# Performance work log

Measured on AMD Instinct MI355X. Metric: run time of the kernel, lower is better.

Reference implementation:

```python
import jax, jax.numpy as jnp
import numpy as np
from jax import lax

B = 65536

def _conv3(x, w, b):
    # x: [B,Cin,H,W], w: [Cout,Cin,3,3] (OIHW), SAME padding, stride 1
    y = lax.conv_general_dilated(x, w, (1, 1), 'SAME',
                                 dimension_numbers=('NCHW', 'OIHW', 'NCHW'))
    return y + b[None, :, None, None]

def _gru_cell(x, h, wu, bu, wr, br, wo, bo):
    s = jnp.concatenate([x, h], axis=1)
    update = jax.nn.sigmoid(_conv3(s, wu, bu))
    reset = jax.nn.sigmoid(_conv3(s, wr, br))
    out = jnp.tanh(_conv3(jnp.concatenate([x, h * reset], axis=1), wo, bo))
    return h * (1.0 - update) + out * update

def _mk_cell_params(key, cin, ch):
    ks = jax.random.split(key, 6)
    fan = (cin + ch) * 9
    sc = 1.0 / np.sqrt(fan)
    p = {}
    for i, g in enumerate(['u', 'r', 'o']):
        p['w' + g] = jax.random.normal(ks[2 * i], (ch, cin + ch, 3, 3), jnp.float32) * sc
        p['b' + g] = jax.random.normal(ks[2 * i + 1], (ch,), jnp.float32) * sc
    return p

def setup_inputs() -> dict:
    key = jax.random.key(0)
    k_in, k1, k2, k3, kd1, kd2 = jax.random.split(key, 6)
    inputs = jax.random.normal(k_in, (B, 1, 3, 3), jnp.float32)
    p1 = _mk_cell_params(k1, 1, 32)
    p2 = _mk_cell_params(k2, 32, 64)
    p3 = _mk_cell_params(k3, 64, 16)
    wd = jax.random.normal(kd1, (9, 16 * 3 * 3), jnp.float32) * (1.0 / 12.0)
    bd = jax.random.normal(kd2, (9,), jnp.float32) * (1.0 / 12.0)
    out = {'inputs': inputs, 'wd': wd, 'bd': bd}
    for i, p in enumerate([p1, p2, p3], start=1):
        for k, v in p.items():
            out[f'{k[0]}{i}{k[1]}'] = v  # e.g. w1u, b1u
    return out

def reference(inputs, wd, bd,
              w1u, b1u, w1r, b1r, w1o, b1o,
              w2u, b2u, w2r, b2r, w2o, b2o,
              w3u, b3u, w3r, b3r, w3o, b3o):
    b = inputs.shape[0]
    h1 = jnp.zeros((b, 32, 3, 3), inputs.dtype)
    h2 = jnp.zeros((b, 64, 3, 3), inputs.dtype)
    h3 = jnp.zeros((b, 16, 3, 3), inputs.dtype)
    x1 = _gru_cell(inputs, h1, w1u, b1u, w1r, b1r, w1o, b1o)
    x2 = _gru_cell(x1, h2, w2u, b2u, w2r, b2r, w2o, b2o)
    x3 = _gru_cell(x2, h3, w3u, b3u, w3r, b3r, w3o, b3o)
    out = x3.reshape(b, -1) @ wd.T + bd
    return (out, x1, x2, x3)
```

## Files before the change

### kernel.cpp

```cpp
#include <hip/hip_runtime.h>

#define BATCH 65536

typedef __attribute__((ext_vector_type(8))) short bf16x8;
typedef __attribute__((ext_vector_type(4))) float f32x4;

__device__ __forceinline__ unsigned short f2bf(float f) {
  unsigned int u = __float_as_uint(f);
  u += 0x7fffu + ((u >> 16) & 1u);
  return (unsigned short)(u >> 16);
}
__device__ __forceinline__ unsigned pack_trunc(float lo, float hi) {
  return __builtin_amdgcn_perm(__float_as_uint(hi), __float_as_uint(lo), 0x07060302u);
}

__device__ __forceinline__ float gru_act(float u, float o) {
  u = fmaxf(u, -60.0f);
  o = fmaxf(o, -30.0f);
  float a  = __expf(-u);
  float a2 = __expf(-2.0f * o);
  return (1.0f - a2) * __builtin_amdgcn_rcpf((1.0f + a) * (1.0f + a2));
}

__device__ __forceinline__ float conv_tap(const float* __restrict__ w, int co, int ci,
                                          int p, int q, int CINTOT) {
  int pi = p / 3, pj = p % 3, qi = q / 3, qj = q % 3;
  int di = qi - pi + 1, dj = qj - pj + 1;
  if ((unsigned)di < 3u && (unsigned)dj < 3u)
    return w[((co * CINTOT + ci) * 3 + di) * 3 + dj];
  return 0.0f;
}

__global__ void build_bt(const float* __restrict__ wu, const float* __restrict__ wo,
                         unsigned short* __restrict__ BT, int COUT, int CINX, int CINTOT) {
  int NG = COUT * 9, K = CINX * 9;
  int total = 2 * NG * K;
  int e = blockIdx.x * 256 + threadIdx.x;
  if (e >= total) return;
  int g = e / (NG * K);
  int rem = e - g * (NG * K);
  int n = rem / K, k = rem - n * K;
  BT[e] = f2bf(conv_tap(g ? wo : wu, n / 9, k / 9, n % 9, k % 9, CINTOT));
}

__global__ void build_bt1(const float* __restrict__ wu, const float* __restrict__ wo,
                          unsigned short* __restrict__ BT1) {
  int e = blockIdx.x * 256 + threadIdx.x;
  if (e >= 18432) return;
  int g = e / 9216;
  int rem = e - g * 9216;
  int n = rem / 32, k = rem - n * 32;
  float v = (k < 9) ? conv_tap(g ? wo : wu, n / 9, 0, n % 9, k, 33) : 0.0f;
  BT1[e] = f2bf(v);
}

#define OFF_X1L 0
#define OFF_X3L 0
#define OFF_WL 20480
#define OFF_BLB 25664
#define OFF_BL 40960
#define OFF_XL2 65536
#define OFF_AL 65536
#define SMEM_BYTES 74752

__global__ __launch_bounds__(256, 2) void megafused(
    const float* __restrict__ xin, const unsigned short* __restrict__ BT1,
    const float* __restrict__ b1u, const float* __restrict__ b1o,
    const unsigned short* __restrict__ BT2,
    const float* __restrict__ b2u, const float* __restrict__ b2o,
    const unsigned short* __restrict__ BT3,
    const float* __restrict__ b3u, const float* __restrict__ b3o,
    const float* __restrict__ wd, const float* __restrict__ bd,
    float* __restrict__ x1, float* __restrict__ x2,
    float* __restrict__ x3, float* __restrict__ out) {
  __shared__ __align__(16) char smem[SMEM_BYTES];
  char* x1l = smem + OFF_X1L;
  char* Bl = smem + OFF_BL;
  char* Al = smem + OFF_AL;
  unsigned short* x3l = (unsigned short*)(smem + OFF_X3L);
  float* xl2 = (float*)(smem + OFF_XL2);
  float* wl = (float*)(smem + OFF_WL);
  float* blb = (float*)(smem + OFF_BLB);

  const int tid = threadIdx.x;
  const int lane = tid & 63;
  const int wid = tid >> 6;
  const int lrow = lane & 15;
  const int jc = lane >> 4;
  const int r0 = blockIdx.x * 64;
  const int srow = tid >> 2, spart = tid & 3;

  unsigned toffB2[6];
  int wOffB2[6];
#pragma unroll
  for (int ci = 0; ci < 6; ++ci) {
    int row = ci * 64 + srow;
    int bg = (row < 192) ? row : (384 + row);
    toffB2[ci] = (unsigned)bg * 288u + spart * 8;
    wOffB2[ci] = row * 64 + ((spart ^ ((row >> 1) & 3)) << 4);
  }
  unsigned toffB1[5];
  int wOffG[5];
#pragma unroll
  for (int j = 0; j < 5; ++j) {
    int c = j * 256 + tid;
    if (c < 1152) {
      int row = c >> 2, p = c & 3;
      int g = row >= 144, nloc = row - (g ? 144 : 0);
      toffB1[j] = (unsigned)(g * 288 + nloc) * 32u + p * 8;
      wOffG[j] = row * 64 + ((p ^ ((row >> 1) & 3)) << 4);
    } else {
      toffB1[j] = 0; wOffG[j] = 0;
    }
  }

  for (int c = tid; c < 2304; c += 256) {
    int row = c / 36, col = c - row * 36;
    xl2[c] = (col < 9) ? xin[(size_t)(r0 + row) * 9 + col] : 0.0f;
  }
  bf16x8 pb[5];
#pragma unroll
  for (int j = 0; j < 5; ++j)
    if (j * 256 + tid < 1152) pb[j] = *(const bf16x8*)(BT1 + toffB1[j]);
  __syncthreads();

  bf16x8 afx[4];
#pragma unroll
  for (int m = 0; m < 4; ++m) {
    const float* xr = xl2 + (m * 16 + lrow) * 36 + jc * 8;
    float4 a0 = *(const float4*)xr;
    float4 a1 = *(const float4*)(xr + 4);
    union { uint4 u; bf16x8 v; } cv;
    cv.u.x = pack_trunc(a0.x, a0.y);
    cv.u.y = pack_trunc(a0.z, a0.w);
    cv.u.z = pack_trunc(a1.x, a1.y);
    cv.u.w = pack_trunc(a1.z, a1.w);
    afx[m] = cv.v;
  }
  int rBoffG[2][3];
#pragma unroll
  for (int g = 0; g < 2; ++g)
#pragma unroll
    for (int f = 0; f < 3; ++f) {
      int rb = g * 144 + (wid * 3 + f) * 16 + lrow;
      rBoffG[g][f] = rb * 64 + ((jc ^ ((rb >> 1) & 3)) << 4);
    }

  bf16x8 pf[6];
#pragma unroll
  for (int ch = 0; ch < 2; ++ch) {
#pragma unroll
    for (int j = 0; j < 5; ++j)
      if (j * 256 + tid < 1152) *(bf16x8*)(Bl + wOffG[j]) = pb[j];
    if (ch == 0) {
#pragma unroll
      for (int j = 0; j < 5; ++j)
        if (j * 256 + tid < 1152) pb[j] = *(const bf16x8*)(BT1 + 4608u + toffB1[j]);
    } else {
#pragma unroll
      for (int q = 0; q < 6; ++q) pf[q] = *(const bf16x8*)(BT2 + toffB2[q]);
    }
    __syncthreads();
    if (wid < 3) {
      f32x4 acc[4][2][3] = {};
      bf16x8 bfr[2][3];
#pragma unroll
      for (int g = 0; g < 2; ++g)
#pragma unroll
        for (int f = 0; f < 3; ++f) bfr[g][f] = *(const bf16x8*)(Bl + rBoffG[g][f]);
#pragma unroll
      for (int m = 0; m < 4; ++m)
#pragma unroll
        for (int g = 0; g < 2; ++g)
#pragma unroll
          for (int f = 0; f < 3; ++f)
            acc[m][g][f] = __builtin_amdgcn_mfma_f32_16x16x32_bf16(
                afx[m], bfr[g][f], acc[m][g][f], 0, 0, 0);
#pragma unroll
      for (int m = 0; m < 4; ++m)
#pragma unroll
        for (int f = 0; f < 3; ++f) {
          int n = ch * 144 + (wid * 3 + f) * 16 + lrow;
          float bU = b1u[n / 9], bO = b1o[n / 9];
          f32x4 uv = acc[m][0][f], ov = acc[m][1][f];
#pragma unroll
          for (int t = 0; t < 4; ++t) {
            int r = m * 16 + jc * 4 + t;
            float v = gru_act(uv[t] + bU, ov[t] + bO);
            x1[(size_t)(r0 + r) * 288 + n] = v;
            *(unsigned short*)(x1l + r * 640 + (((n >> 3) ^ (r & 7)) << 4) + (n & 7) * 2) =
                (unsigned short)(__float_as_uint(v) >> 16);
          }
        }
    }
    __syncthreads();
  }

  {
    int rBoff[2][3];
#pragma unroll
    for (int g = 0; g < 2; ++g)
#pragma unroll
      for (int f = 0; f < 3; ++f) {
        int rb = g * 192 + (wid * 3 + f) * 16 + lrow;
        rBoff[g][f] = rb * 64 + ((jc ^ ((rb >> 1) & 3)) << 4);
      }
    const char* aBase[4];
    int aXor[4];
#pragma unroll
    for (int m = 0; m < 4; ++m) {
      int row = m * 16 + lrow;
      aBase[m] = x1l + row * 640;
      aXor[m] = row & 7;
    }

    f32x4 acc[4][2][3] = {};
    for (int s = 0; s < 27; ++s) {
      const int kt = s - (s / 9) * 9;
#pragma unroll
      for (int ci = 0; ci < 6; ++ci) *(bf16x8*)(Bl + wOffB2[ci]) = pf[ci];
      __syncthreads();
      if (s < 26) {
        int ns = s + 1;
        unsigned uoff = (unsigned)(ns / 9) * 55296u + (unsigned)(ns % 9) * 32u;
#pragma unroll
        for (int ci = 0; ci < 6; ++ci)
          pf[ci] = *(const bf16x8*)(BT2 + uoff + toffB2[ci]);
      }
      bf16x8 af[4];
      const int c8 = kt * 4 + jc;
#pragma unroll
      for (int m = 0; m < 4; ++m)
        af[m] = *(const bf16x8*)(aBase[m] + ((c8 ^ aXor[m]) << 4));
      bf16x8 bfr[2][3];
#pragma unroll
      for (int g = 0; g < 2; ++g)
#pragma unroll
        for (int f = 0; f < 3; ++f) bfr[g][f] = *(const bf16x8*)(Bl + rBoff[g][f]);
#pragma unroll
      for (int m = 0; m < 4; ++m)
#pragma unroll
        for (int g = 0; g < 2; ++g)
#pragma unroll
          for (int f = 0; f < 3; ++f)
            acc[m][g][f] = __builtin_amdgcn_mfma_f32_16x16x32_bf16(
                af[m], bfr[g][f], acc[m][g][f], 0, 0, 0);
      if (kt == 8) {
        const int n0 = (s / 9) * 192;
#pragma unroll
        for (int m = 0; m < 4; ++m)
#pragma unroll
          for (int f = 0; f < 3; ++f) {
            int n = n0 + (wid * 3 + f) * 16 + lrow;
            float bU = b2u[n / 9], bO = b2o[n / 9];
            f32x4 uv = acc[m][0][f], ov = acc[m][1][f];
#pragma unroll
            for (int t = 0; t < 4; ++t) {
              int r = r0 + m * 16 + jc * 4 + t;
              x2[(size_t)r * 576 + n] = gru_act(uv[t] + bU, ov[t] + bO);
            }
            acc[m][0][f] = (f32x4){0.f, 0.f, 0.f, 0.f};
            acc[m][1][f] = (f32x4){0.f, 0.f, 0.f, 0.f};
          }
      }
      __syncthreads();
    }
  }
  __syncthreads();

  for (int c = tid; c < 1296; c += 256) wl[c] = wd[c];
  if (tid < 9) blb[tid] = bd[tid];

  {
    unsigned toffB3[5];
#pragma unroll
    for (int j = 0; j < 5; ++j) {
      int c = j * 256 + tid;
      toffB3[j] = (c < 1152) ? ((unsigned)(c >> 2) * 576u + (c & 3) * 8) : 0u;
    }
    const float* pA = x2 + (size_t)(r0 + srow) * 576 + spart * 8;
    char* wAl = Al + srow * 64 + ((spart ^ ((srow >> 1) & 3)) << 4);

    float4 pa0 = *(const float4*)pA;
    float4 pa1 = *(const float4*)(pA + 4);
    bf16x8 pb3[5];
#pragma unroll
    for (int j = 0; j < 5; ++j)
      if (j * 256 + tid < 1152) pb3[j] = *(const bf16x8*)(BT3 + toffB3[j]);

    const char* rA3[4];
#pragma unroll
    for (int m = 0; m < 4; ++m) {
      int row = m * 16 + lrow;
      rA3[m] = Al + row * 64 + ((jc ^ ((row >> 1) & 3)) << 4);
    }

    f32x4 acc[4][2][3] = {};
    for (int kt = 0; kt < 18; ++kt) {
      uint4 h;
      h.x = pack_trunc(pa0.x, pa0.y);
      h.y = pack_trunc(pa0.z, pa0.w);
      h.z = pack_trunc(pa1.x, pa1.y);
      h.w = pack_trunc(pa1.z, pa1.w);
      *(uint4*)wAl = h;
#pragma unroll
      for (int j = 0; j < 5; ++j)
        if (j * 256 + tid < 1152) *(bf16x8*)(Bl + wOffG[j]) = pb3[j];
      __syncthreads();
      if (kt < 17) {
        const float* gp = pA + (kt + 1) * 32;
        pa0 = *(const float4*)gp;
        pa1 = *(const float4*)(gp + 4);
        unsigned uoff = (unsigned)(kt + 1) * 32u;
#pragma unroll
        for (int j = 0; j < 5; ++j)
          if (j * 256 + tid < 1152) pb3[j] = *(const bf16x8*)(BT3 + uoff + toffB3[j]);
      }
      if (wid < 3) {
        bf16x8 af[4];
#pragma unroll
        for (int m = 0; m < 4; ++m) af[m] = *(const bf16x8*)rA3[m];
        bf16x8 bfr[2][3];
#pragma unroll
        for (int g = 0; g < 2; ++g)
#pragma unroll
          for (int f = 0; f < 3; ++f) bfr[g][f] = *(const bf16x8*)(Bl + rBoffG[g][f]);
#pragma unroll
        for (int m = 0; m < 4; ++m)
#pragma unroll
          for (int g = 0; g < 2; ++g)
#pragma unroll
            for (int f = 0; f < 3; ++f)
              acc[m][g][f] = __builtin_amdgcn_mfma_f32_16x16x32_bf16(
                  af[m], bfr[g][f], acc[m][g][f], 0, 0, 0);
      }
      __syncthreads();
    }
    if (wid < 3) {
#pragma unroll
      for (int m = 0; m < 4; ++m)
#pragma unroll
        for (int f = 0; f < 3; ++f) {
          int n = (wid * 3 + f) * 16 + lrow;
          float bU = b3u[n / 9], bO = b3o[n / 9];
          f32x4 uv = acc[m][0][f], ov = acc[m][1][f];
#pragma unroll
          for (int t = 0; t < 4; ++t) {
            int r = m * 16 + jc * 4 + t;
            float v = gru_act(uv[t] + bU, ov[t] + bO);
            x3[(size_t)(r0 + r) * 144 + n] = v;
            x3l[r * 146 + n] = (unsigned short)(__float_as_uint(v) >> 16);
          }
        }
    }
  }
  __syncthreads();

  if (wid < 3) {
    int drow = lane;
    int jb = wid * 3;
    float s0 = blb[jb], s1 = blb[jb + 1], s2 = blb[jb + 2];
    for (int k = 0; k < 144; k += 2) {
      unsigned pr = *(const unsigned*)&x3l[drow * 146 + k];
      float v0 = __uint_as_float(pr << 16);
      float v1 = __uint_as_float(pr & 0xffff0000u);
      const float2 w0 = *(const float2*)&wl[jb * 144 + k];
      const float2 w1 = *(const float2*)&wl[(jb + 1) * 144 + k];
      const float2 w2 = *(const float2*)&wl[(jb + 2) * 144 + k];
      s0 = fmaf(v0, w0.x, s0); s0 = fmaf(v1, w0.y, s0);
      s1 = fmaf(v0, w1.x, s1); s1 = fmaf(v1, w1.y, s1);
      s2 = fmaf(v0, w2.x, s2); s2 = fmaf(v1, w2.y, s2);
    }
    size_t ob = (size_t)(r0 + drow) * 9 + jb;
    out[ob] = s0; out[ob + 1] = s1; out[ob + 2] = s2;
  }
}

extern "C" void kernel_launch(void* const* d_in, const int* in_sizes, int n_in,
                              void* d_out, int out_size, void* d_ws, size_t ws_size,
                              hipStream_t stream) {
  const float* inputs = (const float*)d_in[0];
  const float* wd  = (const float*)d_in[1];
  const float* bd  = (const float*)d_in[2];
  const float* w1u = (const float*)d_in[3];
  const float* b1u = (const float*)d_in[4];
  const float* w1o = (const float*)d_in[7];
  const float* b1o = (const float*)d_in[8];
  const float* w2u = (const float*)d_in[9];
  const float* b2u = (const float*)d_in[10];
  const float* w2o = (const float*)d_in[13];
  const float* b2o = (const float*)d_in[14];
  const float* w3u = (const float*)d_in[15];
  const float* b3u = (const float*)d_in[16];
  const float* w3o = (const float*)d_in[19];
  const float* b3o = (const float*)d_in[20];

  float* out = (float*)d_out;
  float* x1 = out + (size_t)BATCH * 9;
  float* x2 = x1 + (size_t)BATCH * 288;
  float* x3 = x2 + (size_t)BATCH * 576;

  unsigned short* BT2 = (unsigned short*)d_ws;
  unsigned short* BT3 = BT2 + 331776;
  unsigned short* BT1 = BT3 + 165888;

  build_bt<<<1296, 256, 0, stream>>>(w2u, w2o, BT2, 64, 32, 96);
  build_bt<<<648, 256, 0, stream>>>(w3u, w3o, BT3, 16, 64, 80);
  build_bt1<<<72, 256, 0, stream>>>(w1u, w1o, BT1);

  megafused<<<BATCH / 64, 256, 0, stream>>>(inputs, BT1, b1u, b1o, BT2, b2u, b2o,
                                            BT3, b3u, b3o, wd, bd, x1, x2, x3, out);
}
```

Measured before the change: 154.8 us.

## Load layer-2/3 MFMA operands straight from global into registers, drop LDS staging

Layers 2 and 3 now have each wave load its B-fragments (and for layer 3 its A-fragments from x2) directly from global memory into registers. Double-buffered register sets stand in for the cooperative LDS staging, so the per-step __syncthreads barriers go away and the loop is manually unrolled by two. This removes LDS write/read traffic and block-wide sync on every k-step, and shrinks shared memory use. In exchange each wave issues redundant global loads that rely on cache hits, register pressure rises, and layer 3 reads x2 rows again from global memory.

Measured after the change: 187.0 us. 20.8% more time.

```diff
diff --git a/kernel.cpp b/kernel.cpp
--- a/kernel.cpp
+++ b/kernel.cpp
@@ -59,9 +59,70 @@
 #define OFF_WL 20480
 #define OFF_BLB 25664
 #define OFF_BL 40960
-#define OFF_XL2 65536
-#define OFF_AL 65536
-#define SMEM_BYTES 74752
+#define OFF_XL2 59392
+#define SMEM_BYTES 68608
+
+#define L2_STEP(CUR, NXT, LAST) do {                                        \
+    if (!(LAST)) {                                                          \
+      _Pragma("unroll") for (int g_ = 0; g_ < 2; ++g_)                      \
+        _Pragma("unroll") for (int f_ = 0; f_ < 3; ++f_)                    \
+          NXT[g_][f_] = *(const bf16x8*)(BT2 + ldoff + boff[g_][f_]);       \
+      if (ktn == 8) { ktn = 0; ldoff += 55040u; }                           \
+      else { ++ktn; ldoff += 32u; }                                         \
+    }                                                                       \
+    bf16x8 af_[4];                                                          \
+    const int c8_ = kt * 4 + jc;                                            \
+    _Pragma("unroll") for (int m_ = 0; m_ < 4; ++m_)                        \
+      af_[m_] = *(const bf16x8*)(aBase[m_] + ((c8_ ^ aXor[m_]) << 4));      \
+    _Pragma("unroll") for (int m_ = 0; m_ < 4; ++m_)                        \
+      _Pragma("unroll") for (int g_ = 0; g_ < 2; ++g_)                      \
+        _Pragma("unroll") for (int f_ = 0; f_ < 3; ++f_)                    \
+          acc[m_][g_][f_] = __builtin_amdgcn_mfma_f32_16x16x32_bf16(        \
+              af_[m_], CUR[g_][f_], acc[m_][g_][f_], 0, 0, 0);              \
+    if (kt == 8) {                                                          \
+      _Pragma("unroll") for (int m_ = 0; m_ < 4; ++m_)                      \
+        _Pragma("unroll") for (int f_ = 0; f_ < 3; ++f_) {                  \
+          int n_ = n0 + (wid * 3 + f_) * 16 + lrow;                         \
+          float bU_ = b2u[n_ / 9], bO_ = b2o[n_ / 9];                       \
+          f32x4 uv_ = acc[m_][0][f_], ov_ = acc[m_][1][f_];                 \
+          _Pragma("unroll") for (int t_ = 0; t_ < 4; ++t_) {                \
+            int r_ = r0 + m_ * 16 + jc * 4 + t_;                            \
+            x2[(size_t)r_ * 576 + n_] = gru_act(uv_[t_] + bU_, ov_[t_] + bO_); \
+          }                                                                 \
+          acc[m_][0][f_] = (f32x4){0.f, 0.f, 0.f, 0.f};                     \
+          acc[m_][1][f_] = (f32x4){0.f, 0.f, 0.f, 0.f};                     \
+        }                                                                   \
+      kt = 0; n0 += 192;                                                    \
+    } else ++kt;                                                            \
+  } while (0)
+
+#define L3_STEP(CURB, NXTB, LAST) do {                                      \
+    bf16x8 af_[4];                                                          \
+    _Pragma("unroll") for (int m_ = 0; m_ < 4; ++m_) {                      \
+      union { uint4 u; bf16x8 v; } cv_;                                     \
+      cv_.u.x = pack_trunc(pa0[m_].x, pa0[m_].y);                           \
+      cv_.u.y = pack_trunc(pa0[m_].z, pa0[m_].w);                           \
+      cv_.u.z = pack_trunc(pa1[m_].x, pa1[m_].y);                           \
+      cv_.u.w = pack_trunc(pa1[m_].z, pa1[m_].w);                           \
+      af_[m_] = cv_.v;                                                      \
+    }                                                                       \
+    if (!(LAST)) {                                                          \
+      _Pragma("unroll") for (int m_ = 0; m_ < 4; ++m_) {                    \
+        pa0[m_] = *(const float4*)(x2r[m_] + a3off);                        \
+        pa1[m_] = *(const float4*)(x2r[m_] + a3off + 4);                    \
+      }                                                                     \
+      a3off += 32u;                                                         \
+      _Pragma("unroll") for (int g_ = 0; g_ < 2; ++g_)                      \
+        _Pragma("unroll") for (int f_ = 0; f_ < 3; ++f_)                    \
+          NXTB[g_][f_] = *(const bf16x8*)(BT3 + b3ld + b3off[g_][f_]);      \
+      b3ld += 32u;                                                          \
+    }                                                                       \
+    _Pragma("unroll") for (int m_ = 0; m_ < 4; ++m_)                        \
+      _Pragma("unroll") for (int g_ = 0; g_ < 2; ++g_)                      \
+        _Pragma("unroll") for (int f_ = 0; f_ < 3; ++f_)                    \
+          acc[m_][g_][f_] = __builtin_amdgcn_mfma_f32_16x16x32_bf16(        \
+              af_[m_], CURB[g_][f_], acc[m_][g_][f_], 0, 0, 0);             \
+  } while (0)
 
 __global__ __launch_bounds__(256, 2) void megafused(
     const float* __restrict__ xin, const unsigned short* __restrict__ BT1,
@@ -76,7 +137,6 @@
   __shared__ __align__(16) char smem[SMEM_BYTES];
   char* x1l = smem + OFF_X1L;
   char* Bl = smem + OFF_BL;
-  char* Al = smem + OFF_AL;
   unsigned short* x3l = (unsigned short*)(smem + OFF_X3L);
   float* xl2 = (float*)(smem + OFF_XL2);
   float* wl = (float*)(smem + OFF_WL);
@@ -88,17 +148,15 @@
   const int lrow = lane & 15;
   const int jc = lane >> 4;
   const int r0 = blockIdx.x * 64;
-  const int srow = tid >> 2, spart = tid & 3;
-
-  unsigned toffB2[6];
-  int wOffB2[6];
-#pragma unroll
-  for (int ci = 0; ci < 6; ++ci) {
-    int row = ci * 64 + srow;
-    int bg = (row < 192) ? row : (384 + row);
-    toffB2[ci] = (unsigned)bg * 288u + spart * 8;
-    wOffB2[ci] = row * 64 + ((spart ^ ((row >> 1) & 3)) << 4);
-  }
+
+  unsigned boff[2][3];
+#pragma unroll
+  for (int g = 0; g < 2; ++g)
+#pragma unroll
+    for (int f = 0; f < 3; ++f)
+      boff[g][f] = (unsigned)g * 165888u +
+                   (unsigned)(((wid * 3 + f) * 16 + lrow) * 288) + jc * 8;
+
   unsigned toffB1[5];
   int wOffG[5];
 #pragma unroll
@@ -146,7 +204,7 @@
       rBoffG[g][f] = rb * 64 + ((jc ^ ((rb >> 1) & 3)) << 4);
     }
 
-  bf16x8 pf[6];
+  bf16x8 bX[2][3], bY[2][3];
 #pragma unroll
   for (int ch = 0; ch < 2; ++ch) {
 #pragma unroll
@@ -158,7 +216,10 @@
         if (j * 256 + tid < 1152) pb[j] = *(const bf16x8*)(BT1 + 4608u + toffB1[j]);
     } else {
 #pragma unroll
-      for (int q = 0; q < 6; ++q) pf[q] = *(const bf16x8*)(BT2 + toffB2[q]);
+      for (int g = 0; g < 2; ++g)
+#pragma unroll
+        for (int f = 0; f < 3; ++f)
+          bX[g][f] = *(const bf16x8*)(BT2 + boff[g][f]);
     }
     __syncthreads();
     if (wid < 3) {
@@ -197,14 +258,6 @@
   }
 
   {
-    int rBoff[2][3];
-#pragma unroll
-    for (int g = 0; g < 2; ++g)
-#pragma unroll
-      for (int f = 0; f < 3; ++f) {
-        int rb = g * 192 + (wid * 3 + f) * 16 + lrow;
-        rBoff[g][f] = rb * 64 + ((jc ^ ((rb >> 1) & 3)) << 4);
-      }
     const char* aBase[4];
     int aXor[4];
 #pragma unroll
@@ -213,146 +266,70 @@
       aBase[m] = x1l + row * 640;
       aXor[m] = row & 7;
     }
-
     f32x4 acc[4][2][3] = {};
-    for (int s = 0; s < 27; ++s) {
-      const int kt = s - (s / 9) * 9;
-#pragma unroll
-      for (int ci = 0; ci < 6; ++ci) *(bf16x8*)(Bl + wOffB2[ci]) = pf[ci];
-      __syncthreads();
-      if (s < 26) {
-        int ns = s + 1;
-        unsigned uoff = (unsigned)(ns / 9) * 55296u + (unsigned)(ns % 9) * 32u;
-#pragma unroll
-        for (int ci = 0; ci < 6; ++ci)
-          pf[ci] = *(const bf16x8*)(BT2 + uoff + toffB2[ci]);
-      }
-      bf16x8 af[4];
-      const int c8 = kt * 4 + jc;
-#pragma unroll
-      for (int m = 0; m < 4; ++m)
-        af[m] = *(const bf16x8*)(aBase[m] + ((c8 ^ aXor[m]) << 4));
-      bf16x8 bfr[2][3];
-#pragma unroll
-      for (int g = 0; g < 2; ++g)
-#pragma unroll
-        for (int f = 0; f < 3; ++f) bfr[g][f] = *(const bf16x8*)(Bl + rBoff[g][f]);
-#pragma unroll
-      for (int m = 0; m < 4; ++m)
-#pragma unroll
-        for (int g = 0; g < 2; ++g)
-#pragma unroll
-          for (int f = 0; f < 3; ++f)
-            acc[m][g][f] = __builtin_amdgcn_mfma_f32_16x16x32_bf16(
-                af[m], bfr[g][f], acc[m][g][f], 0, 0, 0);
-      if (kt == 8) {
-        const int n0 = (s / 9) * 192;
-#pragma unroll
-        for (int m = 0; m < 4; ++m)
-#pragma unroll
-          for (int f = 0; f < 3; ++f) {
-            int n = n0 + (wid * 3 + f) * 16 + lrow;
-            float bU = b2u[n / 9], bO = b2o[n / 9];
-            f32x4 uv = acc[m][0][f], ov = acc[m][1][f];
-#pragma unroll
-            for (int t = 0; t < 4; ++t) {
-              int r = r0 + m * 16 + jc * 4 + t;
-              x2[(size_t)r * 576 + n] = gru_act(uv[t] + bU, ov[t] + bO);
-            }
-            acc[m][0][f] = (f32x4){0.f, 0.f, 0.f, 0.f};
-            acc[m][1][f] = (f32x4){0.f, 0.f, 0.f, 0.f};
-          }
-      }
-      __syncthreads();
-    }
+    int kt = 0, n0 = 0, ktn = 1;
+    unsigned ldoff = 32u;
+    for (int sp = 0; sp < 13; ++sp) {
+      L2_STEP(bX, bY, false);
+      L2_STEP(bY, bX, false);
+    }
+    L2_STEP(bX, bY, true);
   }
   __syncthreads();
 
   for (int c = tid; c < 1296; c += 256) wl[c] = wd[c];
   if (tid < 9) blb[tid] = bd[tid];
 
-  {
-    unsigned toffB3[5];
-#pragma unroll
-    for (int j = 0; j < 5; ++j) {
-      int c = j * 256 + tid;
-      toffB3[j] = (c < 1152) ? ((unsigned)(c >> 2) * 576u + (c & 3) * 8) : 0u;
-    }
-    const float* pA = x2 + (size_t)(r0 + srow) * 576 + spart * 8;
-    char* wAl = Al + srow * 64 + ((spart ^ ((srow >> 1) & 3)) << 4);
-
-    float4 pa0 = *(const float4*)pA;
-    float4 pa1 = *(const float4*)(pA + 4);
-    bf16x8 pb3[5];
-#pragma unroll
-    for (int j = 0; j < 5; ++j)
-      if (j * 256 + tid < 1152) pb3[j] = *(const bf16x8*)(BT3 + toffB3[j]);
-
-    const char* rA3[4];
+  if (wid < 3) {
+    unsigned b3off[2][3];
+#pragma unroll
+    for (int g = 0; g < 2; ++g)
+#pragma unroll
+      for (int f = 0; f < 3; ++f)
+        b3off[g][f] = (unsigned)g * 82944u +
+                      (unsigned)(((wid * 3 + f) * 16 + lrow) * 576) + jc * 8;
+    const float* x2r[4];
+#pragma unroll
+    for (int m = 0; m < 4; ++m)
+      x2r[m] = x2 + (size_t)(r0 + m * 16 + lrow) * 576 + jc * 8;
+
+    float4 pa0[4], pa1[4];
 #pragma unroll
     for (int m = 0; m < 4; ++m) {
-      int row = m * 16 + lrow;
-      rA3[m] = Al + row * 64 + ((jc ^ ((row >> 1) & 3)) << 4);
-    }
+      pa0[m] = *(const float4*)(x2r[m]);
+      pa1[m] = *(const float4*)(x2r[m] + 4);
+    }
+    bf16x8 bX3[2][3], bY3[2][3];
+#pragma unroll
+    for (int g = 0; g < 2; ++g)
+#pragma unroll
+      for (int f = 0; f < 3; ++f)
+        bX3[g][f] = *(const bf16x8*)(BT3 + b3off[g][f]);
 
     f32x4 acc[4][2][3] = {};
-    for (int kt = 0; kt < 18; ++kt) {
-      uint4 h;
-      h.x = pack_trunc(pa0.x, pa0.y);
-      h.y = pack_trunc(pa0.z, pa0.w);
-      h.z = pack_trunc(pa1.x, pa1.y);
-      h.w = pack_trunc(pa1.z, pa1.w);
-      *(uint4*)wAl = h;
-#pragma unroll
-      for (int j = 0; j < 5; ++j)
-        if (j * 256 + tid < 1152) *(bf16x8*)(Bl + wOffG[j]) = pb3[j];
-      __syncthreads();
-      if (kt < 17) {
-        const float* gp = pA + (kt + 1) * 32;
-        pa0 = *(const float4*)gp;
-        pa1 = *(const float4*)(gp + 4);
-        unsigned uoff = (unsigned)(kt + 1) * 32u;
-#pragma unroll
-        for (int j = 0; j < 5; ++j)
-          if (j * 256 + tid < 1152) pb3[j] = *(const bf16x8*)(BT3 + uoff + toffB3[j]);
+    unsigned a3off = 32u, b3ld = 32u;
+    for (int sp = 0; sp < 8; ++sp) {
+      L3_STEP(bX3, bY3, false);
+      L3_STEP(bY3, bX3, false);
+    }
+    L3_STEP(bX3, bY3, false);
+    L3_STEP(bY3, bX3, true);
+
+#pragma unroll
+    for (int m = 0; m < 4; ++m)
+#pragma unroll
+      for (int f = 0; f < 3; ++f) {
+        int n = (wid * 3 + f) * 16 + lrow;
+        float bU = b3u[n / 9], bO = b3o[n / 9];
+        f32x4 uv = acc[m][0][f], ov = acc[m][1][f];
+#pragma unroll
+        for (int t = 0; t < 4; ++t) {
+          int r = m * 16 + jc * 4 + t;
+          float v = gru_act(uv[t] + bU, ov[t] + bO);
+          x3[(size_t)(r0 + r) * 144 + n] = v;
+          x3l[r * 146 + n] = (unsigned short)(__float_as_uint(v) >> 16);
+        }
       }
-      if (wid < 3) {
-        bf16x8 af[4];
-#pragma unroll
-        for (int m = 0; m < 4; ++m) af[m] = *(const bf16x8*)rA3[m];
-        bf16x8 bfr[2][3];
-#pragma unroll
-        for (int g = 0; g < 2; ++g)
-#pragma unroll
-          for (int f = 0; f < 3; ++f) bfr[g][f] = *(const bf16x8*)(Bl + rBoffG[g][f]);
-#pragma unroll
-        for (int m = 0; m < 4; ++m)
-#pragma unroll
-          for (int g = 0; g < 2; ++g)
-#pragma unroll
-            for (int f = 0; f < 3; ++f)
-              acc[m][g][f] = __builtin_amdgcn_mfma_f32_16x16x32_bf16(
-                  af[m], bfr[g][f], acc[m][g][f], 0, 0, 0);
-      }
-      __syncthreads();
-    }
-    if (wid < 3) {
-#pragma unroll
-      for (int m = 0; m < 4; ++m)
-#pragma unroll
-        for (int f = 0; f < 3; ++f) {
-          int n = (wid * 3 + f) * 16 + lrow;
-          float bU = b3u[n / 9], bO = b3o[n / 9];
-          f32x4 uv = acc[m][0][f], ov = acc[m][1][f];
-#pragma unroll
-          for (int t = 0; t < 4; ++t) {
-            int r = m * 16 + jc * 4 + t;
-            float v = gru_act(uv[t] + bU, ov[t] + bO);
-            x3[(size_t)(r0 + r) * 144 + n] = v;
-            x3l[r * 146 + n] = (unsigned short)(__float_as_uint(v) >> 16);
-          }
-        }
-    }
   }
   __syncthreads();
 
```

## Halve batch rows per block to raise occupancy to three blocks per CU

Applied to the files above, without the earlier changes.

Cuts the rows handled by each workgroup from 64 to 32, which shrinks the shared-memory footprint and the accumulator register arrays, and raises the launch bound to 3 blocks per CU with twice as many blocks. The goal is better latency hiding through higher occupancy. The cost is that every block must still stream the full weight matrices (BT1/BT2/BT3) from global/L2, so weight traffic per output row doubles and MFMA work per B-fragment load halves. The final dense layer is also remapped so all 256 threads compute one output each, with an extra pass for the ninth output.

Measured after the change: 196.9 us. 1.27x slower.

```diff
diff --git a/kernel.cpp b/kernel.cpp
--- a/kernel.cpp
+++ b/kernel.cpp
@@ -56,14 +56,14 @@
 
 #define OFF_X1L 0
 #define OFF_X3L 0
-#define OFF_WL 20480
-#define OFF_BLB 25664
-#define OFF_BL 40960
-#define OFF_XL2 65536
-#define OFF_AL 65536
-#define SMEM_BYTES 74752
-
-__global__ __launch_bounds__(256, 2) void megafused(
+#define OFF_WL 9344
+#define OFF_BLB 14528
+#define OFF_BL 20480
+#define OFF_XL2 45056
+#define OFF_AL 45056
+#define SMEM_BYTES 49664
+
+__global__ __launch_bounds__(256, 3) void megafused(
     const float* __restrict__ xin, const unsigned short* __restrict__ BT1,
     const float* __restrict__ b1u, const float* __restrict__ b1o,
     const unsigned short* __restrict__ BT2,
@@ -87,7 +87,7 @@
   const int wid = tid >> 6;
   const int lrow = lane & 15;
   const int jc = lane >> 4;
-  const int r0 = blockIdx.x * 64;
+  const int r0 = blockIdx.x * 32;
   const int srow = tid >> 2, spart = tid & 3;
 
   unsigned toffB2[6];
@@ -114,7 +114,7 @@
     }
   }
 
-  for (int c = tid; c < 2304; c += 256) {
+  for (int c = tid; c < 1152; c += 256) {
     int row = c / 36, col = c - row * 36;
     xl2[c] = (col < 9) ? xin[(size_t)(r0 + row) * 9 + col] : 0.0f;
   }
@@ -124,9 +124,9 @@
     if (j * 256 + tid < 1152) pb[j] = *(const bf16x8*)(BT1 + toffB1[j]);
   __syncthreads();
 
-  bf16x8 afx[4];
-#pragma unroll
-  for (int m = 0; m < 4; ++m) {
+  bf16x8 afx[2];
+#pragma unroll
+  for (int m = 0; m < 2; ++m) {
     const float* xr = xl2 + (m * 16 + lrow) * 36 + jc * 8;
     float4 a0 = *(const float4*)xr;
     float4 a1 = *(const float4*)(xr + 4);
@@ -162,14 +162,14 @@
     }
     __syncthreads();
     if (wid < 3) {
-      f32x4 acc[4][2][3] = {};
+      f32x4 acc[2][2][3] = {};
       bf16x8 bfr[2][3];
 #pragma unroll
       for (int g = 0; g < 2; ++g)
 #pragma unroll
         for (int f = 0; f < 3; ++f) bfr[g][f] = *(const bf16x8*)(Bl + rBoffG[g][f]);
 #pragma unroll
-      for (int m = 0; m < 4; ++m)
+      for (int m = 0; m < 2; ++m)
 #pragma unroll
         for (int g = 0; g < 2; ++g)
 #pragma unroll
@@ -177,7 +177,7 @@
             acc[m][g][f] = __builtin_amdgcn_mfma_f32_16x16x32_bf16(
                 afx[m], bfr[g][f], acc[m][g][f], 0, 0, 0);
 #pragma unroll
-      for (int m = 0; m < 4; ++m)
+      for (int m = 0; m < 2; ++m)
 #pragma unroll
         for (int f = 0; f < 3; ++f) {
           int n = ch * 144 + (wid * 3 + f) * 16 + lrow;
@@ -205,16 +205,16 @@
         int rb = g * 192 + (wid * 3 + f) * 16 + lrow;
         rBoff[g][f] = rb * 64 + ((jc ^ ((rb >> 1) & 3)) << 4);
       }
-    const char* aBase[4];
-    int aXor[4];
-#pragma unroll
-    for (int m = 0; m < 4; ++m) {
+    const char* aBase[2];
+    int aXor[2];
+#pragma unroll
+    for (int m = 0; m < 2; ++m) {
       int row = m * 16 + lrow;
       aBase[m] = x1l + row * 640;
       aXor[m] = row & 7;
     }
 
-    f32x4 acc[4][2][3] = {};
+    f32x4 acc[2][2][3] = {};
     for (int s = 0; s < 27; ++s) {
       const int kt = s - (s / 9) * 9;
 #pragma unroll
@@ -227,10 +227,10 @@
         for (int ci = 0; ci < 6; ++ci)
           pf[ci] = *(const bf16x8*)(BT2 + uoff + toffB2[ci]);
       }
-      bf16x8 af[4];
+      bf16x8 af[2];
       const int c8 = kt * 4 + jc;
 #pragma unroll
-      for (int m = 0; m < 4; ++m)
+      for (int m = 0; m < 2; ++m)
         af[m] = *(const bf16x8*)(aBase[m] + ((c8 ^ aXor[m]) << 4));
       bf16x8 bfr[2][3];
 #pragma unroll
@@ -238,7 +238,7 @@
 #pragma unroll
         for (int f = 0; f < 3; ++f) bfr[g][f] = *(const bf16x8*)(Bl + rBoff[g][f]);
 #pragma unroll
-      for (int m = 0; m < 4; ++m)
+      for (int m = 0; m < 2; ++m)
 #pragma unroll
         for (int g = 0; g < 2; ++g)
 #pragma unroll
@@ -248,7 +248,7 @@
       if (kt == 8) {
         const int n0 = (s / 9) * 192;
 #pragma unroll
-        for (int m = 0; m < 4; ++m)
+        for (int m = 0; m < 2; ++m)
 #pragma unroll
           for (int f = 0; f < 3; ++f) {
             int n = n0 + (wid * 3 + f) * 16 + lrow;
@@ -278,55 +278,63 @@
       int c = j * 256 + tid;
       toffB3[j] = (c < 1152) ? ((unsigned)(c >> 2) * 576u + (c & 3) * 8) : 0u;
     }
-    const float* pA = x2 + (size_t)(r0 + srow) * 576 + spart * 8;
-    char* wAl = Al + srow * 64 + ((spart ^ ((srow >> 1) & 3)) << 4);
-
-    float4 pa0 = *(const float4*)pA;
-    float4 pa1 = *(const float4*)(pA + 4);
+    const int arow = tid >> 2;
+    const float* pA = x2 + (size_t)(r0 + arow) * 576 + spart * 8;
+    char* wAl = Al + arow * 64 + ((spart ^ ((arow >> 1) & 3)) << 4);
+
+    float4 pa0 = {}, pa1 = {};
+    if (tid < 128) {
+      pa0 = *(const float4*)pA;
+      pa1 = *(const float4*)(pA + 4);
+    }
     bf16x8 pb3[5];
 #pragma unroll
     for (int j = 0; j < 5; ++j)
       if (j * 256 + tid < 1152) pb3[j] = *(const bf16x8*)(BT3 + toffB3[j]);
 
-    const char* rA3[4];
-#pragma unroll
-    for (int m = 0; m < 4; ++m) {
+    const char* rA3[2];
+#pragma unroll
+    for (int m = 0; m < 2; ++m) {
       int row = m * 16 + lrow;
       rA3[m] = Al + row * 64 + ((jc ^ ((row >> 1) & 3)) << 4);
     }
 
-    f32x4 acc[4][2][3] = {};
+    f32x4 acc[2][2][3] = {};
     for (int kt = 0; kt < 18; ++kt) {
-      uint4 h;
-      h.x = pack_trunc(pa0.x, pa0.y);
-      h.y = pack_trunc(pa0.z, pa0.w);
-      h.z = pack_trunc(pa1.x, pa1.y);
-      h.w = pack_trunc(pa1.z, pa1.w);
-      *(uint4*)wAl = h;
+      if (tid < 128) {
+        uint4 h;
+        h.x = pack_trunc(pa0.x, pa0.y);
+        h.y = pack_trunc(pa0.z, pa0.w);
+        h.z = pack_trunc(pa1.x, pa1.y);
+        h.w = pack_trunc(pa1.z, pa1.w);
+        *(uint4*)wAl = h;
+      }
 #pragma unroll
       for (int j = 0; j < 5; ++j)
         if (j * 256 + tid < 1152) *(bf16x8*)(Bl + wOffG[j]) = pb3[j];
       __syncthreads();
       if (kt < 17) {
-        const float* gp = pA + (kt + 1) * 32;
-        pa0 = *(const float4*)gp;
-        pa1 = *(const float4*)(gp + 4);
+        if (tid < 128) {
+          const float* gp = pA + (kt + 1) * 32;
+          pa0 = *(const float4*)gp;
+          pa1 = *(const float4*)(gp + 4);
+        }
         unsigned uoff = (unsigned)(kt + 1) * 32u;
 #pragma unroll
         for (int j = 0; j < 5; ++j)
           if (j * 256 + tid < 1152) pb3[j] = *(const bf16x8*)(BT3 + uoff + toffB3[j]);
       }
       if (wid < 3) {
-        bf16x8 af[4];
-#pragma unroll
-        for (int m = 0; m < 4; ++m) af[m] = *(const bf16x8*)rA3[m];
+        bf16x8 af[2];
+#pragma unroll
+        for (int m = 0; m < 2; ++m) af[m] = *(const bf16x8*)rA3[m];
         bf16x8 bfr[2][3];
 #pragma unroll
         for (int g = 0; g < 2; ++g)
 #pragma unroll
           for (int f = 0; f < 3; ++f) bfr[g][f] = *(const bf16x8*)(Bl + rBoffG[g][f]);
 #pragma unroll
-        for (int m = 0; m < 4; ++m)
+        for (int m = 0; m < 2; ++m)
 #pragma unroll
           for (int g = 0; g < 2; ++g)
 #pragma unroll
@@ -338,7 +346,7 @@
     }
     if (wid < 3) {
 #pragma unroll
-      for (int m = 0; m < 4; ++m)
+      for (int m = 0; m < 2; ++m)
 #pragma unroll
         for (int f = 0; f < 3; ++f) {
           int n = (wid * 3 + f) * 16 + lrow;
@@ -356,23 +364,31 @@
   }
   __syncthreads();
 
-  if (wid < 3) {
-    int drow = lane;
-    int jb = wid * 3;
-    float s0 = blb[jb], s1 = blb[jb + 1], s2 = blb[jb + 2];
+  {
+    int r = tid & 31;
+    int j = tid >> 5;
+    float s = blb[j];
     for (int k = 0; k < 144; k += 2) {
-      unsigned pr = *(const unsigned*)&x3l[drow * 146 + k];
+      unsigned pr = *(const unsigned*)&x3l[r * 146 + k];
       float v0 = __uint_as_float(pr << 16);
       float v1 = __uint_as_float(pr & 0xffff0000u);
-      const float2 w0 = *(const float2*)&wl[jb * 144 + k];
-      const float2 w1 = *(const float2*)&wl[(jb + 1) * 144 + k];
-      const float2 w2 = *(const float2*)&wl[(jb + 2) * 144 + k];
-      s0 = fmaf(v0, w0.x, s0); s0 = fmaf(v1, w0.y, s0);
-      s1 = fmaf(v0, w1.x, s1); s1 = fmaf(v1, w1.y, s1);
-      s2 = fmaf(v0, w2.x, s2); s2 = fmaf(v1, w2.y, s2);
-    }
-    size_t ob = (size_t)(r0 + drow) * 9 + jb;
-    out[ob] = s0; out[ob + 1] = s1; out[ob + 2] = s2;
+      const float2 w0 = *(const float2*)&wl[j * 144 + k];
+      s = fmaf(v0, w0.x, s);
+      s = fmaf(v1, w0.y, s);
+    }
+    out[(size_t)(r0 + r) * 9 + j] = s;
+    if (tid < 32) {
+      float s8 = blb[8];
+      for (int k = 0; k < 144; k += 2) {
+        unsigned pr = *(const unsigned*)&x3l[r * 146 + k];
+        float v0 = __uint_as_float(pr << 16);
+        float v1 = __uint_as_float(pr & 0xffff0000u);
+        const float2 w0 = *(const float2*)&wl[8 * 144 + k];
+        s8 = fmaf(v0, w0.x, s8);
+        s8 = fmaf(v1, w0.y, s8);
+      }
+      out[(size_t)(r0 + r) * 9 + 8] = s8;
+    }
   }
 }
 
@@ -408,6 +424,6 @@
   build_bt<<<648, 256, 0, stream>>>(w3u, w3o, BT3, 16, 64, 80);
   build_bt1<<<72, 256, 0, stream>>>(w1u, w1o, BT1);
 
-  megafused<<<BATCH / 64, 256, 0, stream>>>(inputs, BT1, b1u, b1o, BT2, b2u, b2o,
+  megafused<<<BATCH / 32, 256, 0, stream>>>(inputs, BT1, b1u, b1o, BT2, b2u, b2o,
                                             BT3, b3u, b3o, wd, bd, x1, x2, x3, out);
 }
```
